# Optimization experiments

Measured on AMD Instinct MI355X. Metric: run time of the kernel, lower is better.

## Reference

```python
import jax, jax.numpy as jnp
import numpy as np

N_POINTS = 1048576
N_LEVELS = 16
F = 2
BASE_RES = 16
FINEST_RES = 512
LOG2_HASH = 19
SIZES = [2 ** min(i + 1, LOG2_HASH) for i in range(N_LEVELS)]  # per-level table rows (powers of 2)
OFFS = np.concatenate([[0], np.cumsum(SIZES)]).astype(np.int64)  # static row offsets into packed table
TOTAL_ROWS = int(OFFS[-1])  # 131070
# hash primes from the torch module; uint32 wraparound matches int64 low-bit behavior
# because each table size is a power of two <= 2^19 < 2^32, so h % 2^k == low k bits.
P0, P1, P2, P3 = np.uint32(1), np.uint32(2654435761), np.uint32(29675113), np.uint32(123456789)
CORNERS = np.array([[0,0,0],[1,0,0],[0,1,0],[1,1,0],
                    [0,0,1],[1,0,1],[0,1,1],[1,1,1]], dtype=np.uint32)  # torch stacking order


def setup_inputs() -> dict:
    key = jax.random.key(0)
    k1, k2 = jax.random.split(key)
    coords = jax.random.uniform(k1, (N_POINTS, 3), dtype=jnp.float32, minval=-1.0, maxval=1.0)
    hash_init_scale = 0.001
    table = jax.random.uniform(k2, (TOTAL_ROWS, F), dtype=jnp.float32,
                               minval=-hash_init_scale, maxval=hash_init_scale)
    return {"coords": coords, "table": table}


def _encode(coords, table):
    corners = jnp.asarray(CORNERS)  # [8,3] uint32
    outs = []
    for level in range(N_LEVELS):
        res = min(BASE_RES * (2 ** level), FINEST_RES)
        cs = (coords + 1.0) * res           # [N,3]
        cf = jnp.floor(cs)
        frac = cs - cf                      # [N,3]
        base = cf.astype(jnp.uint32)        # coords >= -1 so floor >= 0
        c = base[None, :, :] + corners[:, None, :]   # [8,N,3]
        x, y, z = c[..., 0], c[..., 1], c[..., 2]
        h = x * P0
        h = h * P1 + y
        h = h * P2 + z
        h = h * P3
        h = (h & jnp.uint32(SIZES[level] - 1)).astype(jnp.int32)  # mod power-of-2 table size
        feats = table[int(OFFS[level]) + h]          # [8,N,F] gather
        tx = frac[..., 0:1]; ty = frac[..., 1:2]; tz = frac[..., 2:3]
        f = (feats[0] * (1 - tx) * (1 - ty) * (1 - tz)
             + feats[1] * tx * (1 - ty) * (1 - tz)
             + feats[2] * (1 - tx) * ty * (1 - tz)
             + feats[3] * tx * ty * (1 - tz)
             + feats[4] * (1 - tx) * (1 - ty) * tz
             + feats[5] * tx * (1 - ty) * tz
             + feats[6] * (1 - tx) * ty * tz
             + feats[7] * tx * ty * tz)              # [N,F]
        outs.append(f)
    return jnp.concatenate(outs, axis=-1)            # [N, N_LEVELS*F]


def reference(coords, table):
    return _encode(coords, table)
```

## Files before the change

### kernel.cpp

```cpp
#include <hip/hip_runtime.h>
#include <hip/hip_fp16.h>


#define N_POINTS 1048576
#define BLOCK 1024
#define NBLOCKS 512
#define ITERS 16
#define STAGED_ROWS 8190
#define TBL_LDS_BYTES 32768
#define LDS_BYTES (TBL_LDS_BYTES + 128 * 8 * 16)

__device__ __forceinline__ float2 ldsRow(const unsigned* lds, unsigned idx) {
    unsigned u = lds[idx];
    __half2 h = *(__half2*)&u;
    return __half22float2(h);
}

#define PREP(FRES, HARR, WARR) \
    unsigned HARR[8]; float WARR[8]; { \
        const float csx = (px + 1.0f) * (FRES); \
        const float csy = (py + 1.0f) * (FRES); \
        const float csz = (pz + 1.0f) * (FRES); \
        const float cfx = floorf(csx), cfy = floorf(csy), cfz = floorf(csz); \
        const float tx = csx - cfx, ty = csy - cfy, tz = csz - cfz; \
        const unsigned hh = (unsigned)cfx * HA + (unsigned)cfy * HB + (unsigned)cfz * HC; \
        const float ux = 1.0f - tx, uy = 1.0f - ty, uz = 1.0f - tz; \
        WARR[0] = ux*uy*uz; WARR[1] = tx*uy*uz; WARR[2] = ux*ty*uz; WARR[3] = tx*ty*uz; \
        WARR[4] = ux*uy*tz; WARR[5] = tx*uy*tz; WARR[6] = ux*ty*tz; WARR[7] = tx*ty*tz; \
        HARR[0] = hh;           HARR[1] = hh + HA;           \
        HARR[2] = hh + HB;      HARR[3] = hh + HA + HB;      \
        HARR[4] = hh + HC;      HARR[5] = hh + HA + HC;      \
        HARR[6] = hh + HB + HC; HARR[7] = hh + HA + HB + HC; \
    }

#define GATHER_LDS(HARR, WARR, MASK, OFF, O0, O1) \
    { _Pragma("unroll") for (int c = 0; c < 8; ++c) { \
        float2 f = ldsRow(lds_tb, (OFF) + ((HARR[c]) & (MASK))); \
        (O0) += f.x * WARR[c]; (O1) += f.y * WARR[c]; } }

#define GATHER_GBL(HARR, WARR, MASK, OFF, O0, O1) \
    { _Pragma("unroll") for (int c = 0; c < 8; ++c) { \
        float2 f = tb[(OFF) + ((HARR[c]) & (MASK))]; \
        (O0) += f.x * WARR[c]; (O1) += f.y * WARR[c]; } }

__global__ __launch_bounds__(BLOCK) void ngp_encode_kernel(
    const float* __restrict__ coords,
    const float* __restrict__ table,
    float* __restrict__ out)
{
    extern __shared__ unsigned char lds_raw[];
    unsigned* lds_tb = (unsigned*)lds_raw;
    float4* lds_out  = (float4*)(lds_raw + TBL_LDS_BYTES);

    {
        const float4* __restrict__ t4 = (const float4*)table;
        uint2* __restrict__ l2 = (uint2*)lds_tb;
        for (int r = threadIdx.x; r < STAGED_ROWS / 2; r += BLOCK) {
            float4 v = t4[r];
            __half2 a = __floats2half2_rn(v.x, v.y);
            __half2 b = __floats2half2_rn(v.z, v.w);
            uint2 u;
            u.x = *(unsigned*)&a;
            u.y = *(unsigned*)&b;
            l2[r] = u;
        }
    }
    __syncthreads();

    constexpr unsigned P1 = 2654435761u, P2 = 29675113u, P3 = 123456789u;
    constexpr unsigned HA = P1 * P2 * P3;
    constexpr unsigned HB = P2 * P3;
    constexpr unsigned HC = P3;

    const float2* __restrict__ tb = (const float2*)table;
    float4* __restrict__ out4 = (float4*)out;

    const int wv   = __builtin_amdgcn_readfirstlane((int)(threadIdx.x >> 6));
    const int q    = wv & 7;
    const int g    = wv >> 3;
    const int lane = threadIdx.x & 63;
    const int pl   = g * 64 + lane;

    const int l0 = 2 * q;
    const unsigned mask0 = (2u << l0) - 1u, off0 = mask0 - 1u;
    const unsigned mask1 = (4u << l0) - 1u, off1 = mask1 - 1u;

    for (int it = 0; it < ITERS; ++it) {
        const int pbase = blockIdx.x * (ITERS * 128) + it * 128;
        const int p = pbase + pl;

        const float px = coords[3 * p + 0];
        const float py = coords[3 * p + 1];
        const float pz = coords[3 * p + 2];

        float o00 = 0.0f, o01 = 0.0f, o10 = 0.0f, o11 = 0.0f;

        if (q >= 6) {
            PREP(512.0f, hc, wc)
            GATHER_GBL(hc, wc, mask0, off0, o00, o01)
            GATHER_GBL(hc, wc, mask1, off1, o10, o11)
        } else if (q >= 3) {
            PREP(512.0f, hc, wc)
            GATHER_LDS(hc, wc, mask0, off0, o00, o01)
            GATHER_LDS(hc, wc, mask1, off1, o10, o11)
        } else {
            const float fres0 = (float)(16 << l0);
            const float fres1 = (float)(32 << l0);
            {
                PREP(fres0, hA, wA)
                GATHER_LDS(hA, wA, mask0, off0, o00, o01)
            }
            {
                PREP(fres1, hB, wB)
                GATHER_LDS(hB, wB, mask1, off1, o10, o11)
            }
        }

        lds_out[pl * 8 + (q ^ (pl & 7))] = make_float4(o00, o01, o10, o11);
        __syncthreads();
        {
            const int j = threadIdx.x;
            const int lp = j >> 3, qq = j & 7;
            float4 v = lds_out[lp * 8 + (qq ^ (lp & 7))];
            out4[(size_t)pbase * 8 + j] = v;
        }
        __syncthreads();
    }
}

extern "C" void kernel_launch(void* const* d_in, const int* in_sizes, int n_in,
                              void* d_out, int out_size, void* d_ws, size_t ws_size,
                              hipStream_t stream) {
    const float* coords = (const float*)d_in[0];
    const float* table  = (const float*)d_in[1];
    float* out = (float*)d_out;

    hipFuncSetAttribute((const void*)ngp_encode_kernel,
                        hipFuncAttributeMaxDynamicSharedMemorySize,
                        LDS_BYTES);

    ngp_encode_kernel<<<NBLOCKS, BLOCK, LDS_BYTES, stream>>>(coords, table, out);
}
```

Baseline: 269.0 us.

## Pair coarse and fine levels per wave and stage more table rows in LDS

Doubles the fp16 table staging in LDS to cover levels 0-12 and changes the wave-to-level mapping so each wave handles level q and level 15-q. Only waves 0-2 now read levels 13-15 from global memory, one level each, so global gathers are spread across more waves. The output transpose now stores per-level float2 values with an XOR swizzle and reassembles them into float4 writes. The cost is twice the LDS footprint and a larger staging prologue per block, plus an uneven per-wave workload mix.

After: 226.2 us. 1.19x faster.

```diff
diff --git a/kernel.cpp b/kernel.cpp
--- a/kernel.cpp
+++ b/kernel.cpp
@@ -2,13 +2,12 @@
 #include <hip/hip_fp16.h>
 
 
-#define N_POINTS 1048576
 #define BLOCK 1024
 #define NBLOCKS 512
 #define ITERS 16
-#define STAGED_ROWS 8190
-#define TBL_LDS_BYTES 32768
-#define LDS_BYTES (TBL_LDS_BYTES + 128 * 8 * 16)
+#define STAGED_ROWS 16382
+#define TBL_LDS_BYTES 65536
+#define LDS_BYTES (TBL_LDS_BYTES + 16 * 128 * 8)
 
 __device__ __forceinline__ float2 ldsRow(const unsigned* lds, unsigned idx) {
     unsigned u = lds[idx];
@@ -50,7 +49,7 @@
 {
     extern __shared__ unsigned char lds_raw[];
     unsigned* lds_tb = (unsigned*)lds_raw;
-    float4* lds_out  = (float4*)(lds_raw + TBL_LDS_BYTES);
+    float2* lds_t = (float2*)(lds_raw + TBL_LDS_BYTES);
 
     {
         const float4* __restrict__ t4 = (const float4*)table;
@@ -81,9 +80,10 @@
     const int lane = threadIdx.x & 63;
     const int pl   = g * 64 + lane;
 
-    const int l0 = 2 * q;
-    const unsigned mask0 = (2u << l0) - 1u, off0 = mask0 - 1u;
-    const unsigned mask1 = (4u << l0) - 1u, off1 = mask1 - 1u;
+    const int lA = q;
+    const int lB = 15 - q;
+    const unsigned maskA = (2u << lA) - 1u, offA = maskA - 1u;
+    const unsigned maskB = (2u << lB) - 1u, offB = maskB - 1u;
 
     for (int it = 0; it < ITERS; ++it) {
         const int pbase = blockIdx.x * (ITERS * 128) + it * 128;
@@ -93,36 +93,43 @@
         const float py = coords[3 * p + 1];
         const float pz = coords[3 * p + 2];
 
-        float o00 = 0.0f, o01 = 0.0f, o10 = 0.0f, o11 = 0.0f;
+        float oA0 = 0.0f, oA1 = 0.0f, oB0 = 0.0f, oB1 = 0.0f;
 
-        if (q >= 6) {
-            PREP(512.0f, hc, wc)
-            GATHER_GBL(hc, wc, mask0, off0, o00, o01)
-            GATHER_GBL(hc, wc, mask1, off1, o10, o11)
-        } else if (q >= 3) {
-            PREP(512.0f, hc, wc)
-            GATHER_LDS(hc, wc, mask0, off0, o00, o01)
-            GATHER_LDS(hc, wc, mask1, off1, o10, o11)
-        } else {
-            const float fres0 = (float)(16 << l0);
-            const float fres1 = (float)(32 << l0);
+        if (q < 3) {
             {
-                PREP(fres0, hA, wA)
-                GATHER_LDS(hA, wA, mask0, off0, o00, o01)
+                PREP(512.0f, hB, wB)
+                GATHER_GBL(hB, wB, maskB, offB, oB0, oB1)
             }
             {
-                PREP(fres1, hB, wB)
-                GATHER_LDS(hB, wB, mask1, off1, o10, o11)
+                const float fresA = (float)(16 << lA);
+                PREP(fresA, hA, wA)
+                GATHER_LDS(hA, wA, maskA, offA, oA0, oA1)
             }
+        } else if (q < 5) {
+            {
+                const float fresA = (float)(16 << lA);
+                PREP(fresA, hA, wA)
+                GATHER_LDS(hA, wA, maskA, offA, oA0, oA1)
+            }
+            {
+                PREP(512.0f, hB, wB)
+                GATHER_LDS(hB, wB, maskB, offB, oB0, oB1)
+            }
+        } else {
+            PREP(512.0f, hc, wc)
+            GATHER_LDS(hc, wc, maskA, offA, oA0, oA1)
+            GATHER_LDS(hc, wc, maskB, offB, oB0, oB1)
         }
 
-        lds_out[pl * 8 + (q ^ (pl & 7))] = make_float4(o00, o01, o10, o11);
+        lds_t[lA * 128 + (pl ^ (lA & 14))] = make_float2(oA0, oA1);
+        lds_t[lB * 128 + (pl ^ (lB & 14))] = make_float2(oB0, oB1);
         __syncthreads();
         {
-            const int j = threadIdx.x;
+            const int j  = threadIdx.x;
             const int lp = j >> 3, qq = j & 7;
-            float4 v = lds_out[lp * 8 + (qq ^ (lp & 7))];
-            out4[(size_t)pbase * 8 + j] = v;
+            float2 a = lds_t[(2 * qq + 0) * 128 + (lp ^ (2 * qq))];
+            float2 b = lds_t[(2 * qq + 1) * 128 + (lp ^ (2 * qq))];
+            out4[(size_t)pbase * 8 + j] = make_float4(a.x, a.y, b.x, b.y);
         }
         __syncthreads();
     }
```

## Stage levels 0-13 in LDS and map level pairs to adjacent lanes

Applied to the files above, without the earlier changes.

Enlarges the LDS staging of the hash table from the first 8190 rows to 32766 rows (levels 0-13, as fp16), so only the last level pair is read from global memory. Work assignment changes from one level pair per wave to one level pair per lane, with 8 adjacent lanes covering one point. Each thread can then write its float4 of output directly in coalesced order, which removes the LDS transpose buffer and both per-iteration barriers. The costs are a much larger LDS staging phase per block and 128 KB of LDS per block, which may limit occupancy. Branches now diverge within a wave, since one lane in eight takes the global-gather path, and every thread computes two PREPs even where the levels coincide.

Result: faster. 239.6 us (-10.9%).

```diff
diff --git a/kernel.cpp b/kernel.cpp
--- a/kernel.cpp
+++ b/kernel.cpp
@@ -2,13 +2,11 @@
 #include <hip/hip_fp16.h>
 
 
-#define N_POINTS 1048576
 #define BLOCK 1024
 #define NBLOCKS 512
 #define ITERS 16
-#define STAGED_ROWS 8190
-#define TBL_LDS_BYTES 32768
-#define LDS_BYTES (TBL_LDS_BYTES + 128 * 8 * 16)
+#define STAGED_ROWS 32766
+#define LDS_BYTES 131072
 
 __device__ __forceinline__ float2 ldsRow(const unsigned* lds, unsigned idx) {
     unsigned u = lds[idx];
@@ -48,9 +46,7 @@
     const float* __restrict__ table,
     float* __restrict__ out)
 {
-    extern __shared__ unsigned char lds_raw[];
-    unsigned* lds_tb = (unsigned*)lds_raw;
-    float4* lds_out  = (float4*)(lds_raw + TBL_LDS_BYTES);
+    extern __shared__ unsigned lds_tb[];
 
     {
         const float4* __restrict__ t4 = (const float4*)table;
@@ -75,56 +71,34 @@
     const float2* __restrict__ tb = (const float2*)table;
     float4* __restrict__ out4 = (float4*)out;
 
-    const int wv   = __builtin_amdgcn_readfirstlane((int)(threadIdx.x >> 6));
-    const int q    = wv & 7;
-    const int g    = wv >> 3;
-    const int lane = threadIdx.x & 63;
-    const int pl   = g * 64 + lane;
-
+    const int q = threadIdx.x & 7;
     const int l0 = 2 * q;
     const unsigned mask0 = (2u << l0) - 1u, off0 = mask0 - 1u;
     const unsigned mask1 = (4u << l0) - 1u, off1 = mask1 - 1u;
+    const float fres0 = (l0 < 5) ? (float)(16 << l0) : 512.0f;
+    const float fres1 = (l0 < 4) ? (float)(32 << l0) : 512.0f;
 
     for (int it = 0; it < ITERS; ++it) {
-        const int pbase = blockIdx.x * (ITERS * 128) + it * 128;
-        const int p = pbase + pl;
+        const int t = (blockIdx.x * ITERS + it) * BLOCK + threadIdx.x;
+        const int p = t >> 3;
 
         const float px = coords[3 * p + 0];
         const float py = coords[3 * p + 1];
         const float pz = coords[3 * p + 2];
 
-        float o00 = 0.0f, o01 = 0.0f, o10 = 0.0f, o11 = 0.0f;
+        PREP(fres0, h0, w0)
+        PREP(fres1, h1, w1)
 
-        if (q >= 6) {
-            PREP(512.0f, hc, wc)
-            GATHER_GBL(hc, wc, mask0, off0, o00, o01)
-            GATHER_GBL(hc, wc, mask1, off1, o10, o11)
-        } else if (q >= 3) {
-            PREP(512.0f, hc, wc)
-            GATHER_LDS(hc, wc, mask0, off0, o00, o01)
-            GATHER_LDS(hc, wc, mask1, off1, o10, o11)
+        float o0 = 0.0f, o1 = 0.0f, o2 = 0.0f, o3 = 0.0f;
+        if (q != 7) {
+            GATHER_LDS(h0, w0, mask0, off0, o0, o1)
+            GATHER_LDS(h1, w1, mask1, off1, o2, o3)
         } else {
-            const float fres0 = (float)(16 << l0);
-            const float fres1 = (float)(32 << l0);
-            {
-                PREP(fres0, hA, wA)
-                GATHER_LDS(hA, wA, mask0, off0, o00, o01)
-            }
-            {
-                PREP(fres1, hB, wB)
-                GATHER_LDS(hB, wB, mask1, off1, o10, o11)
-            }
+            GATHER_GBL(h0, w0, mask0, off0, o0, o1)
+            GATHER_GBL(h1, w1, mask1, off1, o2, o3)
         }
 
-        lds_out[pl * 8 + (q ^ (pl & 7))] = make_float4(o00, o01, o10, o11);
-        __syncthreads();
-        {
-            const int j = threadIdx.x;
-            const int lp = j >> 3, qq = j & 7;
-            float4 v = lds_out[lp * 8 + (qq ^ (lp & 7))];
-            out4[(size_t)pbase * 8 + j] = v;
-        }
-        __syncthreads();
+        out4[t] = make_float4(o0, o1, o2, o3);
     }
 }
 
```
